# Performance work log

Hardware: AMD Instinct MI355X
Metric: run time of the kernel (lower is better)

## Reference

```python
import jax, jax.numpy as jnp
import numpy as np

N, D, DFF, E, TOPK = 32768, 256, 1024, 8, 2


def setup_inputs() -> dict:
    key = jax.random.key(0)
    ks = jax.random.split(key, 5)
    return {
        "x": jax.random.normal(ks[0], (N, D), dtype=jnp.float32),
        "gate_w": jax.random.normal(ks[1], (D, E), dtype=jnp.float32) * 0.02,
        "gate_b": jnp.zeros((E,), jnp.float32),
        "w1": jax.random.normal(ks[2], (E, D, DFF), dtype=jnp.float32) * 0.02,
        "b1": jnp.zeros((E, DFF), jnp.float32),
        "w2": jax.random.normal(ks[3], (E, DFF, D), dtype=jnp.float32) * 0.02,
        "b2": jnp.zeros((E, D), jnp.float32),
        "top_k": TOPK,
    }


def reference(x, gate_w, gate_b, w1, b1, w2, b2, top_k):
    # Gating network: linear -> softmax -> top-k (returns topk_vals, topk_idx)
    logits = x @ gate_w + gate_b                       # [N, E]
    probs = jax.nn.softmax(logits, axis=-1)
    topk_vals, topk_idx = jax.lax.top_k(probs, top_k)  # [N, K], [N, K]

    # Naive full-batch expert evaluation (every expert runs on every token),
    # faithful to the original loop that applies the selected expert to all of x.
    h = jax.nn.relu(jnp.einsum('nd,edf->enf', x, w1) + b1[:, None, :])  # [E, N, DFF]
    y = jnp.einsum('enf,efd->end', h, w2) + b2[:, None, :]              # [E, N, D]

    # Per-token gather of the top-k experts' outputs, then weighted sum.
    y = jnp.transpose(y, (1, 0, 2))                                      # [N, E, D]
    sel = jnp.take_along_axis(y, topk_idx[:, :, None], axis=1)           # [N, K, D]
    return jnp.sum(sel * topk_vals[:, :, None], axis=1)                  # [N, D]
```

## Files before the change

### kernel.cpp

```cpp
#include <hip/hip_runtime.h>

#define N_TOK 32768
#define D 256
#define DFF 1024
#define NE 8
#define TB 64

typedef __attribute__((ext_vector_type(16))) float f32x16;
typedef __attribute__((ext_vector_type(8)))  short bf16x8;

#define BARRIER() do {                                        \
    asm volatile("s_waitcnt lgkmcnt(0)" ::: "memory");        \
    __builtin_amdgcn_s_barrier();                             \
    __builtin_amdgcn_sched_barrier(0);                        \
} while (0)

__device__ __forceinline__ unsigned short f2bf(float f) {
    union { float f; unsigned u; } v; v.f = f;
    unsigned r = v.u + 0x7FFFu + ((v.u >> 16) & 1u);
    return (unsigned short)(r >> 16);
}

__global__ __launch_bounds__(256) void wf_prep(
    const float* __restrict__ w1, const float* __restrict__ w2,
    short* __restrict__ w1f, short* __restrict__ w2f) {
    const int b = blockIdx.x;
    if (b < 1024) {
        const int gid  = b * 256 + threadIdx.x;
        const int lane = gid & 63;
        const int frag = gid >> 6;
        const int dblk = frag & 15;
        const int fblk = (frag >> 4) & 31;
        const int e    = frag >> 9;
        const int l31 = lane & 31, g = lane >> 5;

        const float* src = w1 + ((size_t)e * 256 + dblk * 16 + g * 8) * 1024
                              + fblk * 32 + l31;
        unsigned u[4];
#pragma unroll
        for (int jp = 0; jp < 4; ++jp) {
            float a = src[(size_t)(jp * 2)     * 1024];
            float c = src[(size_t)(jp * 2 + 1) * 1024];
            u[jp] = (unsigned)f2bf(a) | ((unsigned)f2bf(c) << 16);
        }
        *(uint4*)(w1f + (size_t)gid * 8) = make_uint4(u[0], u[1], u[2], u[3]);
    } else {
        const int gid  = (b - 1024) * 256 + threadIdx.x;
        const int lane = gid & 63;
        const int frag = gid >> 6;
        const int fblk = frag & 63;
        const int cblk = (frag >> 6) & 7;
        const int e    = frag >> 9;
        const int l31 = lane & 31, g = lane >> 5;

        const float* src = w2 + ((size_t)e * 1024 + fblk * 16 + g * 8) * 256
                              + cblk * 32 + l31;
        unsigned u[4];
#pragma unroll
        for (int jp = 0; jp < 4; ++jp) {
            float a = src[(size_t)(jp * 2)     * 256];
            float c = src[(size_t)(jp * 2 + 1) * 256];
            u[jp] = (unsigned)f2bf(a) | ((unsigned)f2bf(c) << 16);
        }
        *(uint4*)(w2f + (size_t)gid * 8) = make_uint4(u[0], u[1], u[2], u[3]);
    }
}

__global__ __launch_bounds__(256) void gate_all(
    const float* __restrict__ x, const float* __restrict__ gw,
    const float* __restrict__ gb,
    int* __restrict__ cnt, int* __restrict__ bidx, float* __restrict__ bp,
    int2* __restrict__ opos) {
    __shared__ float gws[2048];
    __shared__ int   se1[256], se2[256];
    __shared__ float sp1[256], sp2[256];
    __shared__ int   hist[NE], base_[NE];

    const int tid = threadIdx.x;
#pragma unroll
    for (int i = 0; i < 8; ++i) gws[tid + 256 * i] = gw[tid + 256 * i];
    if (tid < NE) hist[tid] = 0;
    __syncthreads();

    const int t = blockIdx.x * 256 + tid;
    const float* xr = x + (size_t)t * D;

    double acc[NE];
#pragma unroll
    for (int e = 0; e < NE; ++e) acc[e] = 0.0;

    for (int d0 = 0; d0 < 256; d0 += 4) {
        float4 xv = *(const float4*)(xr + d0);
        float xa[4] = {xv.x, xv.y, xv.z, xv.w};
#pragma unroll
        for (int j = 0; j < 4; ++j) {
            float4 ga  = *(const float4*)&gws[(d0 + j) * 8];
            float4 gbb = *(const float4*)&gws[(d0 + j) * 8 + 4];
            double xd = (double)xa[j];
            acc[0] += xd * (double)ga.x;  acc[1] += xd * (double)ga.y;
            acc[2] += xd * (double)ga.z;  acc[3] += xd * (double)ga.w;
            acc[4] += xd * (double)gbb.x; acc[5] += xd * (double)gbb.y;
            acc[6] += xd * (double)gbb.z; acc[7] += xd * (double)gbb.w;
        }
    }

    double l[NE];
#pragma unroll
    for (int e = 0; e < NE; ++e) l[e] = acc[e] + (double)gb[e];
    int e1 = 0;
#pragma unroll
    for (int e = 1; e < NE; ++e) if (l[e] > l[e1]) e1 = e;
    int e2 = (e1 == 0) ? 1 : 0;
#pragma unroll
    for (int e = 0; e < NE; ++e) if (e != e1 && l[e] > l[e2]) e2 = e;

    double s = 0.0;
#pragma unroll
    for (int e = 0; e < NE; ++e) s += exp(l[e] - l[e1]);
    se1[tid] = e1; se2[tid] = e2;
    sp1[tid] = (float)(1.0 / s);
    sp2[tid] = (float)(exp(l[e2] - l[e1]) / s);
    __syncthreads();

    const int pos1 = atomicAdd(&hist[se1[tid]], 1);
    const int pos2 = atomicAdd(&hist[se2[tid]], 1);
    __syncthreads();
    if (tid < NE) base_[tid] = atomicAdd(&cnt[tid], hist[tid]);
    __syncthreads();

    const int o1 = se1[tid] * N_TOK + base_[se1[tid]] + pos1;
    const int o2 = se2[tid] * N_TOK + base_[se2[tid]] + pos2;
    bidx[o1] = t;  bp[o1] = sp1[tid];
    bidx[o2] = t;  bp[o2] = sp2[tid];
    opos[t] = make_int2(o1, o2);
}

__global__ __launch_bounds__(256, 2) void expert_ffn(
    const float* __restrict__ x,
    const short* __restrict__ w1f,
    const short* __restrict__ w2f,
    const float* __restrict__ b1, const float* __restrict__ b2,
    const int* __restrict__ cnt, const int* __restrict__ bidx,
    const float* __restrict__ bp, float* __restrict__ out,
    float* __restrict__ yp, int staged) {
    const int e    = blockIdx.x & 7;
    const int tile = blockIdx.x >> 3;
    const int n_e  = cnt[e];
    const int row0 = tile * TB;
    if (row0 >= n_e) return;

    __shared__ short xs[16 * 64 * 16];
    __shared__ short hs[2][16 * 512];
    __shared__ int   tok_s[TB];
    __shared__ float p_s[TB];

    const int tid  = threadIdx.x;
    const int lane = tid & 63, wid = tid >> 6;
    const int l31  = lane & 31, g = lane >> 5;

    if (tid < TB) {
        int r = row0 + tid;
        tok_s[tid] = (r < n_e) ? bidx[e * N_TOK + r] : -1;
        p_s[tid]   = (r < n_e) ? bp[e * N_TOK + r] : 0.f;
    }
    BARRIER();

    {
        const int tok = tid >> 2;
        const int tk  = tok_s[tok];
        const float* xrow = x + (size_t)(tk < 0 ? 0 : tk) * D;
#pragma unroll
        for (int i = 0; i < 4; ++i) {
            const int dblk = (tid & 3) * 4 + i;
            unsigned u[8];
            if (tk >= 0) {
#pragma unroll
                for (int q = 0; q < 4; ++q) {
                    float4 v = *(const float4*)(xrow + dblk * 16 + q * 4);
                    u[q * 2 + 0] = (unsigned)f2bf(v.x) | ((unsigned)f2bf(v.y) << 16);
                    u[q * 2 + 1] = (unsigned)f2bf(v.z) | ((unsigned)f2bf(v.w) << 16);
                }
            } else {
#pragma unroll
                for (int q = 0; q < 8; ++q) u[q] = 0;
            }
            short* dp = &xs[dblk * 1024 + tok * 16];
            *(uint4*)(dp)     = make_uint4(u[0], u[1], u[2], u[3]);
            *(uint4*)(dp + 8) = make_uint4(u[4], u[5], u[6], u[7]);
        }
    }

    f32x16 acc[2][2];
#pragma unroll
    for (int a = 0; a < 2; ++a)
#pragma unroll
        for (int b = 0; b < 2; ++b)
#pragma unroll
            for (int r = 0; r < 16; ++r) acc[a][b][r] = 0.f;

    const short* w1e = w1f + (size_t)e * (32 * 16 * 512);
    const short* w2e = w2f + (size_t)e * (8 * 64 * 512);
    const float* b1e = b1 + e * DFF;

    bf16x8 w1pre[8];
    {
        const short* w1p0 = w1e + ((size_t)(0 * 4 + wid) * 16) * 512 + lane * 8;
#pragma unroll
        for (int k = 0; k < 8; ++k) w1pre[k] = *(const bf16x8*)(w1p0 + k * 512);
    }

    BARRIER();

    for (int fc = 0; fc < 8; ++fc) {
        const short* w1c = w1e + ((size_t)(fc * 4 + wid) * 16) * 512 + lane * 8;

        bf16x8 w1hi[8];
#pragma unroll
        for (int k = 0; k < 8; ++k) w1hi[k] = *(const bf16x8*)(w1c + (k + 8) * 512);

        f32x16 h0, h1;
#pragma unroll
        for (int r = 0; r < 16; ++r) { h0[r] = 0.f; h1[r] = 0.f; }

        __builtin_amdgcn_s_setprio(1);
        {
            bf16x8 xc0 = *(const bf16x8*)&xs[l31 * 16 + g * 8];
            bf16x8 xc1 = *(const bf16x8*)&xs[512 + l31 * 16 + g * 8];
            bf16x8 xn0 = *(const bf16x8*)&xs[1024 + l31 * 16 + g * 8];
            bf16x8 xn1 = *(const bf16x8*)&xs[1024 + 512 + l31 * 16 + g * 8];
#pragma unroll
            for (int db = 0; db < 16; ++db) {
                bf16x8 f0 = xc0, f1 = xc1;
                xc0 = xn0; xc1 = xn1;
                if (db < 14) {
                    xn0 = *(const bf16x8*)&xs[(db + 2) * 1024 + l31 * 16 + g * 8];
                    xn1 = *(const bf16x8*)&xs[(db + 2) * 1024 + 512 + l31 * 16 + g * 8];
                }
                const bf16x8 w = (db < 8) ? w1pre[db] : w1hi[db - 8];
                h0 = __builtin_amdgcn_mfma_f32_32x32x16_bf16(w, f0, h0, 0, 0, 0);
                h1 = __builtin_amdgcn_mfma_f32_32x32x16_bf16(w, f1, h1, 0, 0, 0);
            }
        }
        __builtin_amdgcn_s_setprio(0);

        const short* w2p = w2e + ((size_t)(wid * 2) * 64 + fc * 8) * 512 + lane * 8;
        bf16x8 wb[4][2];
#pragma unroll
        for (int fb = 0; fb < 4; ++fb) {
            wb[fb][0] = *(const bf16x8*)(w2p + fb * 512);
            wb[fb][1] = *(const bf16x8*)(w2p + fb * 512 + (size_t)64 * 512);
        }

        if (fc < 7) {
            const short* w1n = w1e + ((size_t)((fc + 1) * 4 + wid) * 16) * 512 + lane * 8;
#pragma unroll
            for (int k = 0; k < 8; ++k) w1pre[k] = *(const bf16x8*)(w1n + k * 512);
        }

        short* hbuf = &hs[fc & 1][0];
#pragma unroll
        for (int th = 0; th < 2; ++th) {
            const f32x16& hh = th ? h1 : h0;
#pragma unroll
            for (int m = 0; m < 4; ++m) {
                float4 bq = *(const float4*)(b1e + fc * 128 + wid * 32 + 8 * m + 4 * g);
                float v0 = fmaxf(hh[4 * m + 0] + bq.x, 0.f);
                float v1 = fmaxf(hh[4 * m + 1] + bq.y, 0.f);
                float v2 = fmaxf(hh[4 * m + 2] + bq.z, 0.f);
                float v3 = fmaxf(hh[4 * m + 3] + bq.w, 0.f);
                uint2 pk;
                pk.x = (unsigned)f2bf(v0) | ((unsigned)f2bf(v1) << 16);
                pk.y = (unsigned)f2bf(v2) | ((unsigned)f2bf(v3) << 16);
                const int fragid = (2 * wid + (m >> 1)) * 2 + th;
                *(uint2*)&hbuf[fragid * 512 + ((m & 1) * 32 + l31) * 8 + 4 * g] = pk;
            }
        }

        BARRIER();

        __builtin_amdgcn_s_setprio(1);
        {
            bf16x8 hc0 = *(const bf16x8*)&hbuf[0 * 512 + lane * 8];
            bf16x8 hc1 = *(const bf16x8*)&hbuf[1 * 512 + lane * 8];
            bf16x8 wr[4][2];
#pragma unroll
            for (int fb = 0; fb < 8; ++fb) {
                bf16x8 a0 = hc0, a1 = hc1;
                if (fb < 7) {
                    hc0 = *(const bf16x8*)&hbuf[(2 * fb + 2) * 512 + lane * 8];
                    hc1 = *(const bf16x8*)&hbuf[(2 * fb + 3) * 512 + lane * 8];
                }
                bf16x8 wA, wB;
                if (fb < 4) {
                    wA = wb[fb][0]; wB = wb[fb][1];
                    wr[fb][0] = *(const bf16x8*)(w2p + (fb + 4) * 512);
                    wr[fb][1] = *(const bf16x8*)(w2p + (fb + 4) * 512 + (size_t)64 * 512);
                } else {
                    wA = wr[fb - 4][0]; wB = wr[fb - 4][1];
                }
                acc[0][0] = __builtin_amdgcn_mfma_f32_32x32x16_bf16(a0, wA, acc[0][0], 0, 0, 0);
                acc[0][1] = __builtin_amdgcn_mfma_f32_32x32x16_bf16(a0, wB, acc[0][1], 0, 0, 0);
                acc[1][0] = __builtin_amdgcn_mfma_f32_32x32x16_bf16(a1, wA, acc[1][0], 0, 0, 0);
                acc[1][1] = __builtin_amdgcn_mfma_f32_32x32x16_bf16(a1, wB, acc[1][1], 0, 0, 0);
            }
        }
        __builtin_amdgcn_s_setprio(0);
    }

    const float* b2e = b2 + e * D;
    if (staged) {
        float* ype = yp + ((size_t)e * N_TOK + row0) * 256;
#pragma unroll
        for (int tp = 0; tp < 2; ++tp) {
#pragma unroll
            for (int cb = 0; cb < 2; ++cb) {
                const int col = wid * 64 + cb * 32 + l31;
                const float bv = b2e[col];
#pragma unroll
                for (int r = 0; r < 16; ++r) {
                    const int tl = tp * 32 + (r & 3) + 8 * (r >> 2) + 4 * g;
                    if (tok_s[tl] >= 0)
                        __builtin_nontemporal_store(
                            (acc[tp][cb][r] + bv) * p_s[tl],
                            &ype[(size_t)tl * 256 + col]);
                }
            }
        }
    } else {
#pragma unroll
        for (int tp = 0; tp < 2; ++tp) {
#pragma unroll
            for (int cb = 0; cb < 2; ++cb) {
                const int col = wid * 64 + cb * 32 + l31;
                const float bv = b2e[col];
#pragma unroll
                for (int r = 0; r < 16; ++r) {
                    const int tl = tp * 32 + (r & 3) + 8 * (r >> 2) + 4 * g;
                    const int tk = tok_s[tl];
                    if (tk >= 0)
                        atomicAdd(out + (size_t)tk * D + col,
                                  (acc[tp][cb][r] + bv) * p_s[tl]);
                }
            }
        }
    }
}

__global__ __launch_bounds__(256) void combine(
    const float* __restrict__ yp, const int2* __restrict__ opos,
    float* __restrict__ out) {
    const int gid   = blockIdx.x * 256 + threadIdx.x;
    const int t     = gid >> 6;
    const int lane4 = gid & 63;
    const int2 o = opos[t];
    const float4 a = ((const float4*)yp)[(size_t)o.x * 64 + lane4];
    const float4 b = ((const float4*)yp)[(size_t)o.y * 64 + lane4];
    float4 r;
    r.x = a.x + b.x; r.y = a.y + b.y; r.z = a.z + b.z; r.w = a.w + b.w;
    ((float4*)out)[gid] = r;
}

extern "C" void kernel_launch(void* const* d_in, const int* in_sizes, int n_in,
                              void* d_out, int out_size, void* d_ws, size_t ws_size,
                              hipStream_t stream) {
    const float* x  = (const float*)d_in[0];
    const float* gw = (const float*)d_in[1];
    const float* gb = (const float*)d_in[2];
    const float* w1 = (const float*)d_in[3];
    const float* b1 = (const float*)d_in[4];
    const float* w2 = (const float*)d_in[5];
    const float* b2 = (const float*)d_in[6];
    float* out = (float*)d_out;

    char* ws = (char*)d_ws;
    size_t off = 0;
    int*   cnt   = (int*)(ws + off);  off += 256;
    int*   bidx  = (int*)(ws + off);  off += (size_t)NE * N_TOK * 4;
    float* bp    = (float*)(ws + off); off += (size_t)NE * N_TOK * 4;
    int2*  opos  = (int2*)(ws + off); off += (size_t)N_TOK * 8;
    short* w1f   = (short*)(ws + off); off += (size_t)NE * D * DFF * 2;
    short* w2f   = (short*)(ws + off); off += (size_t)NE * D * DFF * 2;
    float* yp    = (float*)(ws + off); off += (size_t)2 * N_TOK * D * 4;
    const int staged = (ws_size >= off) ? 1 : 0;

    hipMemsetAsync(cnt, 0, 256, stream);
    if (!staged)
        hipMemsetAsync(d_out, 0, (size_t)out_size * sizeof(float), stream);

    gate_all<<<N_TOK / 256, 256, 0, stream>>>(x, gw, gb, cnt, bidx, bp, opos);
    wf_prep<<<2048, 256, 0, stream>>>(w1, w2, w1f, w2f);
    expert_ffn<<<NE * (N_TOK / TB), 256, 0, stream>>>(x, w1f, w2f, b1, b2,
                                                      cnt, bidx, bp, out, yp, staged);
    if (staged)
        combine<<<(N_TOK * D / 4) / 256, 256, 0, stream>>>(yp, opos, out);
}
```

Baseline: 166.8 us.

## Widen expert FFN blocks to 8 waves and restructure FC chunking

```diff
diff --git a/kernel.cpp b/kernel.cpp
--- a/kernel.cpp
+++ b/kernel.cpp
@@ -135,7 +135,7 @@
     opos[t] = make_int2(o1, o2);
 }
 
-__global__ __launch_bounds__(256, 2) void expert_ffn(
+__global__ __launch_bounds__(512, 4) void expert_ffn(
     const float* __restrict__ x,
     const short* __restrict__ w1f,
     const short* __restrict__ w2f,
@@ -150,7 +150,7 @@
     if (row0 >= n_e) return;
 
     __shared__ short xs[16 * 64 * 16];
-    __shared__ short hs[2][16 * 512];
+    __shared__ short hs[32 * 512];
     __shared__ int   tok_s[TB];
     __shared__ float p_s[TB];
 
@@ -166,12 +166,12 @@
     BARRIER();
 
     {
-        const int tok = tid >> 2;
+        const int tok = tid >> 3;
         const int tk  = tok_s[tok];
         const float* xrow = x + (size_t)(tk < 0 ? 0 : tk) * D;
 #pragma unroll
-        for (int i = 0; i < 4; ++i) {
-            const int dblk = (tid & 3) * 4 + i;
+        for (int i = 0; i < 2; ++i) {
+            const int dblk = (tid & 7) * 2 + i;
             unsigned u[8];
             if (tk >= 0) {
 #pragma unroll
@@ -190,80 +190,52 @@
         }
     }
 
-    f32x16 acc[2][2];
+    f32x16 acc[2];
 #pragma unroll
     for (int a = 0; a < 2; ++a)
 #pragma unroll
-        for (int b = 0; b < 2; ++b)
-#pragma unroll
-            for (int r = 0; r < 16; ++r) acc[a][b][r] = 0.f;
+        for (int r = 0; r < 16; ++r) acc[a][r] = 0.f;
 
     const short* w1e = w1f + (size_t)e * (32 * 16 * 512);
     const short* w2e = w2f + (size_t)e * (8 * 64 * 512);
     const float* b1e = b1 + e * DFF;
 
-    bf16x8 w1pre[8];
-    {
-        const short* w1p0 = w1e + ((size_t)(0 * 4 + wid) * 16) * 512 + lane * 8;
-#pragma unroll
-        for (int k = 0; k < 8; ++k) w1pre[k] = *(const bf16x8*)(w1p0 + k * 512);
-    }
-
     BARRIER();
 
-    for (int fc = 0; fc < 8; ++fc) {
-        const short* w1c = w1e + ((size_t)(fc * 4 + wid) * 16) * 512 + lane * 8;
-
-        bf16x8 w1hi[8];
-#pragma unroll
-        for (int k = 0; k < 8; ++k) w1hi[k] = *(const bf16x8*)(w1c + (k + 8) * 512);
-
+    for (int fc = 0; fc < 4; ++fc) {
         f32x16 h0, h1;
 #pragma unroll
         for (int r = 0; r < 16; ++r) { h0[r] = 0.f; h1[r] = 0.f; }
 
+        const short* w1p = w1e + ((size_t)(fc * 8 + wid) * 16) * 512 + lane * 8;
         __builtin_amdgcn_s_setprio(1);
         {
-            bf16x8 xc0 = *(const bf16x8*)&xs[l31 * 16 + g * 8];
-            bf16x8 xc1 = *(const bf16x8*)&xs[512 + l31 * 16 + g * 8];
-            bf16x8 xn0 = *(const bf16x8*)&xs[1024 + l31 * 16 + g * 8];
-            bf16x8 xn1 = *(const bf16x8*)&xs[1024 + 512 + l31 * 16 + g * 8];
+            bf16x8 a0 = *(const bf16x8*)(w1p);
+            bf16x8 x0 = *(const bf16x8*)&xs[l31 * 16 + g * 8];
+            bf16x8 x1 = *(const bf16x8*)&xs[512 + l31 * 16 + g * 8];
 #pragma unroll
             for (int db = 0; db < 16; ++db) {
-                bf16x8 f0 = xc0, f1 = xc1;
-                xc0 = xn0; xc1 = xn1;
-                if (db < 14) {
-                    xn0 = *(const bf16x8*)&xs[(db + 2) * 1024 + l31 * 16 + g * 8];
-                    xn1 = *(const bf16x8*)&xs[(db + 2) * 1024 + 512 + l31 * 16 + g * 8];
+                bf16x8 an, y0, y1;
+                if (db < 15) {
+                    an = *(const bf16x8*)(w1p + (db + 1) * 512);
+                    y0 = *(const bf16x8*)&xs[(db + 1) * 1024 + l31 * 16 + g * 8];
+                    y1 = *(const bf16x8*)&xs[(db + 1) * 1024 + 512 + l31 * 16 + g * 8];
                 }
-                const bf16x8 w = (db < 8) ? w1pre[db] : w1hi[db - 8];
-                h0 = __builtin_amdgcn_mfma_f32_32x32x16_bf16(w, f0, h0, 0, 0, 0);
-                h1 = __builtin_amdgcn_mfma_f32_32x32x16_bf16(w, f1, h1, 0, 0, 0);
+                h0 = __builtin_amdgcn_mfma_f32_32x32x16_bf16(a0, x0, h0, 0, 0, 0);
+                h1 = __builtin_amdgcn_mfma_f32_32x32x16_bf16(a0, x1, h1, 0, 0, 0);
+                if (db < 15) { a0 = an; x0 = y0; x1 = y1; }
             }
         }
         __builtin_amdgcn_s_setprio(0);
 
-        const short* w2p = w2e + ((size_t)(wid * 2) * 64 + fc * 8) * 512 + lane * 8;
-        bf16x8 wb[4][2];
-#pragma unroll
-        for (int fb = 0; fb < 4; ++fb) {
-            wb[fb][0] = *(const bf16x8*)(w2p + fb * 512);
-            wb[fb][1] = *(const bf16x8*)(w2p + fb * 512 + (size_t)64 * 512);
-        }
-
-        if (fc < 7) {
-            const short* w1n = w1e + ((size_t)((fc + 1) * 4 + wid) * 16) * 512 + lane * 8;
-#pragma unroll
-            for (int k = 0; k < 8; ++k) w1pre[k] = *(const bf16x8*)(w1n + k * 512);
-        }
-
-        short* hbuf = &hs[fc & 1][0];
-#pragma unroll
-        for (int th = 0; th < 2; ++th) {
-            const f32x16& hh = th ? h1 : h0;
+        BARRIER();
+
+#pragma unroll
+        for (int tp = 0; tp < 2; ++tp) {
+            const f32x16& hh = tp ? h1 : h0;
 #pragma unroll
             for (int m = 0; m < 4; ++m) {
-                float4 bq = *(const float4*)(b1e + fc * 128 + wid * 32 + 8 * m + 4 * g);
+                float4 bq = *(const float4*)(b1e + fc * 256 + wid * 32 + 8 * m + 4 * g);
                 float v0 = fmaxf(hh[4 * m + 0] + bq.x, 0.f);
                 float v1 = fmaxf(hh[4 * m + 1] + bq.y, 0.f);
                 float v2 = fmaxf(hh[4 * m + 2] + bq.z, 0.f);
@@ -271,76 +243,62 @@
                 uint2 pk;
                 pk.x = (unsigned)f2bf(v0) | ((unsigned)f2bf(v1) << 16);
                 pk.y = (unsigned)f2bf(v2) | ((unsigned)f2bf(v3) << 16);
-                const int fragid = (2 * wid + (m >> 1)) * 2 + th;
-                *(uint2*)&hbuf[fragid * 512 + ((m & 1) * 32 + l31) * 8 + 4 * g] = pk;
-            }
-        }
+                const int fragid = (2 * wid + (m >> 1)) * 2 + tp;
+                *(uint2*)&hs[fragid * 512 + ((m & 1) * 32 + l31) * 8 + 4 * g] = pk;
+            }
+        }
+
+        const short* w2p = w2e + ((size_t)wid * 64 + fc * 16) * 512 + lane * 8;
+        bf16x8 wcur = *(const bf16x8*)(w2p);
 
         BARRIER();
 
         __builtin_amdgcn_s_setprio(1);
         {
-            bf16x8 hc0 = *(const bf16x8*)&hbuf[0 * 512 + lane * 8];
-            bf16x8 hc1 = *(const bf16x8*)&hbuf[1 * 512 + lane * 8];
-            bf16x8 wr[4][2];
-#pragma unroll
-            for (int fb = 0; fb < 8; ++fb) {
-                bf16x8 a0 = hc0, a1 = hc1;
-                if (fb < 7) {
-                    hc0 = *(const bf16x8*)&hbuf[(2 * fb + 2) * 512 + lane * 8];
-                    hc1 = *(const bf16x8*)&hbuf[(2 * fb + 3) * 512 + lane * 8];
+            bf16x8 ha0 = *(const bf16x8*)&hs[0 * 512 + lane * 8];
+            bf16x8 ha1 = *(const bf16x8*)&hs[1 * 512 + lane * 8];
+#pragma unroll
+            for (int kt = 0; kt < 16; ++kt) {
+                bf16x8 wn, hb0, hb1;
+                if (kt < 15) {
+                    wn  = *(const bf16x8*)(w2p + (kt + 1) * 512);
+                    hb0 = *(const bf16x8*)&hs[((kt + 1) * 2 + 0) * 512 + lane * 8];
+                    hb1 = *(const bf16x8*)&hs[((kt + 1) * 2 + 1) * 512 + lane * 8];
                 }
-                bf16x8 wA, wB;
-                if (fb < 4) {
-                    wA = wb[fb][0]; wB = wb[fb][1];
-                    wr[fb][0] = *(const bf16x8*)(w2p + (fb + 4) * 512);
-                    wr[fb][1] = *(const bf16x8*)(w2p + (fb + 4) * 512 + (size_t)64 * 512);
-                } else {
-                    wA = wr[fb - 4][0]; wB = wr[fb - 4][1];
-                }
-                acc[0][0] = __builtin_amdgcn_mfma_f32_32x32x16_bf16(a0, wA, acc[0][0], 0, 0, 0);
-                acc[0][1] = __builtin_amdgcn_mfma_f32_32x32x16_bf16(a0, wB, acc[0][1], 0, 0, 0);
-                acc[1][0] = __builtin_amdgcn_mfma_f32_32x32x16_bf16(a1, wA, acc[1][0], 0, 0, 0);
-                acc[1][1] = __builtin_amdgcn_mfma_f32_32x32x16_bf16(a1, wB, acc[1][1], 0, 0, 0);
+                acc[0] = __builtin_amdgcn_mfma_f32_32x32x16_bf16(ha0, wcur, acc[0], 0, 0, 0);
+                acc[1] = __builtin_amdgcn_mfma_f32_32x32x16_bf16(ha1, wcur, acc[1], 0, 0, 0);
+                if (kt < 15) { wcur = wn; ha0 = hb0; ha1 = hb1; }
             }
         }
         __builtin_amdgcn_s_setprio(0);
     }
 
     const float* b2e = b2 + e * D;
+    const int col = wid * 32 + l31;
+    const float bv = b2e[col];
     if (staged) {
         float* ype = yp + ((size_t)e * N_TOK + row0) * 256;
 #pragma unroll
         for (int tp = 0; tp < 2; ++tp) {
 #pragma unroll
-            for (int cb = 0; cb < 2; ++cb) {
-                const int col = wid * 64 + cb * 32 + l31;
-                const float bv = b2e[col];
-#pragma unroll
-                for (int r = 0; r < 16; ++r) {
-                    const int tl = tp * 32 + (r & 3) + 8 * (r >> 2) + 4 * g;
-                    if (tok_s[tl] >= 0)
-                        __builtin_nontemporal_store(
-                            (acc[tp][cb][r] + bv) * p_s[tl],
-                            &ype[(size_t)tl * 256 + col]);
-                }
+            for (int r = 0; r < 16; ++r) {
+                const int tl = tp * 32 + (r & 3) + 8 * (r >> 2) + 4 * g;
+                if (tok_s[tl] >= 0)
+                    __builtin_nontemporal_store(
+                        (acc[tp][r] + bv) * p_s[tl],
+                        &ype[(size_t)tl * 256 + col]);
             }
         }
     } else {
 #pragma unroll
         for (int tp = 0; tp < 2; ++tp) {
 #pragma unroll
-            for (int cb = 0; cb < 2; ++cb) {
-                const int col = wid * 64 + cb * 32 + l31;
-                const float bv = b2e[col];
-#pragma unroll
-                for (int r = 0; r < 16; ++r) {
-                    const int tl = tp * 32 + (r & 3) + 8 * (r >> 2) + 4 * g;
-                    const int tk = tok_s[tl];
-                    if (tk >= 0)
-                        atomicAdd(out + (size_t)tk * D + col,
-                                  (acc[tp][cb][r] + bv) * p_s[tl]);
-                }
+            for (int r = 0; r < 16; ++r) {
+                const int tl = tp * 32 + (r & 3) + 8 * (r >> 2) + 4 * g;
+                const int tk = tok_s[tl];
+                if (tk >= 0)
+                    atomicAdd(out + (size_t)tk * D + col,
+                              (acc[tp][r] + bv) * p_s[tl]);
             }
         }
     }
@@ -387,9 +345,9 @@
     if (!staged)
         hipMemsetAsync(d_out, 0, (size_t)out_size * sizeof(float), stream);
 
+    wf_prep<<<2048, 256, 0, stream>>>(w1, w2, w1f, w2f);
     gate_all<<<N_TOK / 256, 256, 0, stream>>>(x, gw, gb, cnt, bidx, bp, opos);
-    wf_prep<<<2048, 256, 0, stream>>>(w1, w2, w1f, w2f);
-    expert_ffn<<<NE * (N_TOK / TB), 256, 0, stream>>>(x, w1f, w2f, b1, b2,
+    expert_ffn<<<NE * (N_TOK / TB), 512, 0, stream>>>(x, w1f, w2f, b1, b2,
                                                       cnt, bidx, bp, out, yp, staged);
     if (staged)
         combine<<<(N_TOK * D / 4) / 256, 256, 0, stream>>>(yp, opos, out);
```

New measurement: 159.9 us. -4.1%, faster.
